# Performance work log

Hardware: AMD Instinct MI355X
Metric: run time of the kernel (lower is better)

## Reference

```python
import jax, jax.numpy as jnp
import numpy as np

NUM_EMB = 16384
EMB_DIM = 64
BETA = 0.25  # commitment_cost, legacy=True formulation


def _l2norm(x, axis=-1):
    # matches F.normalize(p=2): x / max(||x||, 1e-12)
    n = jnp.sqrt(jnp.sum(x * x, axis=axis, keepdims=True))
    return x / jnp.maximum(n, 1e-12)


def setup_inputs() -> dict:
    key = jax.random.key(0)
    k_z, k_cb, k_w, k_b = jax.random.split(key, 4)
    z = jax.random.normal(k_z, (16, 1024, EMB_DIM), dtype=jnp.float32)
    # frozen codebook: N(0, d^{-0.5})
    codebook = jax.random.normal(k_cb, (NUM_EMB, EMB_DIM), dtype=jnp.float32) * (EMB_DIM ** -0.5)
    # Linear(d, d) default init: U(-1/sqrt(d), 1/sqrt(d))
    lim = 1.0 / np.sqrt(EMB_DIM)
    proj_w = jax.random.uniform(k_w, (EMB_DIM, EMB_DIM), dtype=jnp.float32, minval=-lim, maxval=lim)
    proj_b = jax.random.uniform(k_b, (EMB_DIM,), dtype=jnp.float32, minval=-lim, maxval=lim)
    scale = jnp.float32(10.0)  # l2_norm_scale
    return {"z": z, "codebook": codebook, "proj_w": proj_w, "proj_b": proj_b, "scale": scale}


def reference(z, codebook, proj_w, proj_b, scale):
    B, T, d = z.shape
    zf = z.reshape(-1, d)                                   # [BT, d]
    quant_codebook = codebook @ proj_w.T + proj_b           # [N, d]
    zn = _l2norm(zf)
    cn = _l2norm(quant_codebook)
    distances = -jnp.einsum('bd,nd->bn', zn, cn) * scale    # [BT, N]
    idx = jnp.argmin(distances, axis=1)                     # [BT]
    quantized = quant_codebook[idx].reshape(z.shape)        # [B, T, d]
    sg = jax.lax.stop_gradient
    commitment_loss = jnp.mean((sg(quantized) - z) ** 2)
    codebook_loss = jnp.mean((quantized - sg(z)) ** 2)
    vq_loss = commitment_loss + BETA * codebook_loss        # legacy=True
    quantized_st = z + sg(quantized - z)                    # straight-through
    return quantized_st, vq_loss, idx.reshape(B, T)
```

## Files before the change

### kernel.cpp

```cpp
#include <hip/hip_runtime.h>
#include <hip/hip_bf16.h>


#define NCODES 16384
#define NTOK   16384
#define DIM    64
#define MARGIN_MFMA 8e-3f
#define CAP    16

typedef __attribute__((ext_vector_type(8))) short bf16x8;
typedef __attribute__((ext_vector_type(4))) float f32x4;
#define GLOBAL_AS __attribute__((address_space(1)))
#define LDS_AS    __attribute__((address_space(3)))

__device__ float  g_qcb[NCODES * DIM];
__device__ short  g_cnb[NCODES * DIM];
__device__ short  g_znb[NTOK * DIM];
__device__ unsigned g_topu[NTOK];
__device__ int    g_candcnt[NTOK];
__device__ int    g_cand[NTOK * CAP];
__device__ int    g_wl[NTOK];
__device__ int    g_wln;
__device__ float  g_partial[512];

__device__ __forceinline__ float wave_sum64(float v) {
#pragma unroll
  for (int o = 32; o > 0; o >>= 1) v += __shfl_xor(v, o, 64);
  return v;
}
__device__ __forceinline__ short f2bf(float f) {
  __hip_bfloat16 h = __float2bfloat16(f);
  return *reinterpret_cast<short*>(&h);
}
__device__ __forceinline__ float bf2f(short s) {
  __hip_bfloat16 h = *reinterpret_cast<__hip_bfloat16*>(&s);
  return __bfloat162float(h);
}
__device__ __forceinline__ void split8(const float* v, bf16x8& hi, bf16x8& lo) {
#pragma unroll
  for (int i = 0; i < 8; ++i) {
    float f = v[i];
    short h = f2bf(f);
    hi[i] = h;
    lo[i] = f2bf(f - bf2f(h));
  }
}

__global__ __launch_bounds__(256) void k_prep(const float* __restrict__ cb,
                                              const float* __restrict__ pw,
                                              const float* __restrict__ pb,
                                              const float* __restrict__ z) {
  int tid = threadIdx.x;
  int wave = tid >> 6, lane = tid & 63, quad = lane >> 4, col = lane & 15;
  if (blockIdx.x < 256) {
    int rowBase = blockIdx.x * 64 + wave * 16;
    const float* cr = cb + (size_t)(rowBase + col) * 64 + quad * 8;
    bf16x8 ah0, al0, ah1, al1;
    split8(cr, ah0, al0);
    split8(cr + 32, ah1, al1);
    float vals[4][4];
    float nr[4] = {0.f, 0.f, 0.f, 0.f};
    const f32x4 fz = {0.f, 0.f, 0.f, 0.f};
#pragma unroll
    for (int nt = 0; nt < 4; ++nt) {
      int j = col + 16 * nt;
      const float* wr = pw + (size_t)j * 64 + quad * 8;
      bf16x8 bh0, bl0, bh1, bl1;
      split8(wr, bh0, bl0);
      split8(wr + 32, bh1, bl1);
      f32x4 d = __builtin_amdgcn_mfma_f32_16x16x32_bf16(ah0, bh0, fz, 0, 0, 0);
      d = __builtin_amdgcn_mfma_f32_16x16x32_bf16(ah1, bh1, d, 0, 0, 0);
      d = __builtin_amdgcn_mfma_f32_16x16x32_bf16(ah0, bl0, d, 0, 0, 0);
      d = __builtin_amdgcn_mfma_f32_16x16x32_bf16(ah1, bl1, d, 0, 0, 0);
      d = __builtin_amdgcn_mfma_f32_16x16x32_bf16(al0, bh0, d, 0, 0, 0);
      d = __builtin_amdgcn_mfma_f32_16x16x32_bf16(al1, bh1, d, 0, 0, 0);
      float bj = pb[j];
#pragma unroll
      for (int r = 0; r < 4; ++r) {
        float v = d[r] + bj;
        vals[nt][r] = v;
        nr[r] = fmaf(v, v, nr[r]);
      }
    }
#pragma unroll
    for (int r = 0; r < 4; ++r) {
      float v = nr[r];
      v += __shfl_xor(v, 1, 64);
      v += __shfl_xor(v, 2, 64);
      v += __shfl_xor(v, 4, 64);
      v += __shfl_xor(v, 8, 64);
      nr[r] = 1.0f / fmaxf(sqrtf(v), 1e-12f);
    }
#pragma unroll
    for (int nt = 0; nt < 4; ++nt)
#pragma unroll
      for (int r = 0; r < 4; ++r) {
        int row = rowBase + quad * 4 + r;
        int j = col + 16 * nt;
        g_qcb[(size_t)row * 64 + j] = vals[nt][r];
        g_cnb[(size_t)row * 64 + j] = f2bf(vals[nt][r] * nr[r]);
      }
  } else {
    int zb = blockIdx.x - 256;
    int gid = zb * 256 + tid;
    if (gid < NTOK) { g_topu[gid] = 0u; g_candcnt[gid] = 0; }
    if (gid == 0) g_wln = 0;
    int base = zb * 64;
    for (int r = 0; r < 16; ++r) {
      int row = base + wave * 16 + r;
      float v = z[(size_t)row * 64 + lane];
      float tot = wave_sum64(v * v);
      g_znb[(size_t)row * 64 + lane] = f2bf(v / fmaxf(sqrtf(tot), 1e-12f));
    }
  }
}

__global__ __launch_bounds__(256) void k_mfma1() {
  __shared__ __align__(16) short smB[2][8192];
  int tid = threadIdx.x;
  int wave = tid >> 6, lane = tid & 63;
  int quad = lane >> 4, col = lane & 15;
  int tokBlock = blockIdx.x >> 3, split = blockIdx.x & 7;
  int tokBase = tokBlock * 128 + wave * 32;

  const short* za = g_znb + (size_t)(tokBase + col) * 64 + quad * 8;
  bf16x8 A0[2], A1[2];
#pragma unroll
  for (int f = 0; f < 2; ++f) {
    A0[f] = *(const bf16x8*)(za + f * 16 * 64);
    A1[f] = *(const bf16x8*)(za + f * 16 * 64 + 32);
  }
  float m[2][4];
#pragma unroll
  for (int f = 0; f < 2; ++f)
#pragma unroll
    for (int r = 0; r < 4; ++r) m[f][r] = -3.0e38f;

  const char* gsplit = (const char*)(g_cnb + (size_t)split * 2048 * 64);
  int x = col & 7;
  int s0off = ((quad ^ x) << 3);
  int s1off = (((4 | quad) ^ x) << 3);
  int goff[4];
#pragma unroll
  for (int i = 0; i < 4; ++i) {
    int cidx = wave * 256 + i * 64 + lane;
    int row = cidx >> 3, sw = cidx & 7;
    goff[i] = row * 128 + ((sw ^ (row & 7)) << 4);
  }

#pragma unroll
  for (int i = 0; i < 4; ++i)
    __builtin_amdgcn_global_load_lds((const GLOBAL_AS void*)(gsplit + goff[i]),
                                     (LDS_AS void*)(&smB[0][wave * 2048 + i * 512]), 16, 0, 0);
  __syncthreads();

  int p = 0;
  for (int s = 0; s < 16; ++s) {
    if (s < 15) {
      const char* gb = gsplit + (size_t)(s + 1) * 16384;
#pragma unroll
      for (int i = 0; i < 4; ++i)
        __builtin_amdgcn_global_load_lds((const GLOBAL_AS void*)(gb + goff[i]),
                                         (LDS_AS void*)(&smB[p ^ 1][wave * 2048 + i * 512]),
                                         16, 0, 0);
    }
    const short* bufp = smB[p];
#pragma unroll
    for (int h = 0; h < 2; ++h) {
      bf16x8 B0[4], B1[4];
#pragma unroll
      for (int t = 0; t < 4; ++t) {
        const short* lb = bufp + ((h * 4 + t) * 16 + col) * 64;
        B0[t] = *(const bf16x8*)(lb + s0off);
        B1[t] = *(const bf16x8*)(lb + s1off);
      }
#pragma unroll
      for (int t = 0; t < 4; ++t) {
#pragma unroll
        for (int f = 0; f < 2; ++f) {
          f32x4 acc = {0.f, 0.f, 0.f, 0.f};
          acc = __builtin_amdgcn_mfma_f32_16x16x32_bf16(A0[f], B0[t], acc, 0, 0, 0);
          acc = __builtin_amdgcn_mfma_f32_16x16x32_bf16(A1[f], B1[t], acc, 0, 0, 0);
#pragma unroll
          for (int r = 0; r < 4; ++r) m[f][r] = fmaxf(m[f][r], acc[r]);
        }
      }
    }
    __syncthreads();
    p ^= 1;
  }

#pragma unroll
  for (int f = 0; f < 2; ++f)
#pragma unroll
    for (int r = 0; r < 4; ++r) {
      float v = m[f][r];
      v = fmaxf(v, __shfl_xor(v, 1, 64));
      v = fmaxf(v, __shfl_xor(v, 2, 64));
      v = fmaxf(v, __shfl_xor(v, 4, 64));
      v = fmaxf(v, __shfl_xor(v, 8, 64));
      if (col == 0) {
        unsigned b = __float_as_uint(v);
        unsigned e = (b & 0x80000000u) ? ~b : (b | 0x80000000u);
        atomicMax(&g_topu[tokBase + f * 16 + quad * 4 + r], e);
      }
    }
}

__global__ __launch_bounds__(256) void k_mfma2() {
  __shared__ __align__(16) short smB[2][8192];
  int tid = threadIdx.x;
  int wave = tid >> 6, lane = tid & 63;
  int quad = lane >> 4, col = lane & 15;
  int tokBlock = blockIdx.x >> 3, split = blockIdx.x & 7;
  int tokBase = tokBlock * 128 + wave * 32;

  const short* za = g_znb + (size_t)(tokBase + col) * 64 + quad * 8;
  bf16x8 A0[2], A1[2];
#pragma unroll
  for (int f = 0; f < 2; ++f) {
    A0[f] = *(const bf16x8*)(za + f * 16 * 64);
    A1[f] = *(const bf16x8*)(za + f * 16 * 64 + 32);
  }
  float th[2][4];
#pragma unroll
  for (int f = 0; f < 2; ++f)
#pragma unroll
    for (int r = 0; r < 4; ++r) {
      unsigned u = g_topu[tokBase + f * 16 + quad * 4 + r];
      unsigned b = (u & 0x80000000u) ? (u & 0x7FFFFFFFu) : ~u;
      th[f][r] = __uint_as_float(b) - MARGIN_MFMA;
    }

  const char* gsplit = (const char*)(g_cnb + (size_t)split * 2048 * 64);
  int x = col & 7;
  int s0off = ((quad ^ x) << 3);
  int s1off = (((4 | quad) ^ x) << 3);
  int goff[4];
#pragma unroll
  for (int i = 0; i < 4; ++i) {
    int cidx = wave * 256 + i * 64 + lane;
    int row = cidx >> 3, sw = cidx & 7;
    goff[i] = row * 128 + ((sw ^ (row & 7)) << 4);
  }

#pragma unroll
  for (int i = 0; i < 4; ++i)
    __builtin_amdgcn_global_load_lds((const GLOBAL_AS void*)(gsplit + goff[i]),
                                     (LDS_AS void*)(&smB[0][wave * 2048 + i * 512]), 16, 0, 0);
  __syncthreads();

  int codeB = split * 2048 + col;
  int p = 0;
  for (int s = 0; s < 16; ++s) {
    if (s < 15) {
      const char* gb = gsplit + (size_t)(s + 1) * 16384;
#pragma unroll
      for (int i = 0; i < 4; ++i)
        __builtin_amdgcn_global_load_lds((const GLOBAL_AS void*)(gb + goff[i]),
                                         (LDS_AS void*)(&smB[p ^ 1][wave * 2048 + i * 512]),
                                         16, 0, 0);
    }
    const short* bufp = smB[p];
#pragma unroll
    for (int h = 0; h < 2; ++h) {
      bf16x8 B0[4], B1[4];
#pragma unroll
      for (int t = 0; t < 4; ++t) {
        const short* lb = bufp + ((h * 4 + t) * 16 + col) * 64;
        B0[t] = *(const bf16x8*)(lb + s0off);
        B1[t] = *(const bf16x8*)(lb + s1off);
      }
#pragma unroll
      for (int t = 0; t < 4; ++t) {
        int code = codeB + s * 128 + (h * 4 + t) * 16;
#pragma unroll
        for (int f = 0; f < 2; ++f) {
          f32x4 acc = {0.f, 0.f, 0.f, 0.f};
          acc = __builtin_amdgcn_mfma_f32_16x16x32_bf16(A0[f], B0[t], acc, 0, 0, 0);
          acc = __builtin_amdgcn_mfma_f32_16x16x32_bf16(A1[f], B1[t], acc, 0, 0, 0);
          float dmax = fmaxf(fmaxf(acc[0] - th[f][0], acc[1] - th[f][1]),
                             fmaxf(acc[2] - th[f][2], acc[3] - th[f][3]));
          if (dmax >= 0.f) {
#pragma unroll
            for (int r = 0; r < 4; ++r) {
              if (acc[r] >= th[f][r]) {
                int tok = tokBase + f * 16 + quad * 4 + r;
                int pos = atomicAdd(&g_candcnt[tok], 1);
                if (pos < CAP) g_cand[tok * CAP + pos] = code;
              }
            }
          }
        }
      }
    }
    __syncthreads();
    p ^= 1;
  }
}

__global__ __launch_bounds__(256) void k_scan() {
  __shared__ int flags[256];
  __shared__ int sbase;
  int tid = threadIdx.x;
  int tok = blockIdx.x * 256 + tid;
  int flag = (g_candcnt[tok] >= 2) ? 1 : 0;
  flags[tid] = flag;
  __syncthreads();
  if (tid == 0) {
    int run = 0;
    for (int i = 0; i < 256; ++i) {
      int f = flags[i];
      flags[i] = run;
      run += f;
    }
    sbase = atomicAdd(&g_wln, run);
  }
  __syncthreads();
  if (flag) g_wl[sbase + flags[tid]] = tok;
}

__global__ __launch_bounds__(256) void k_arb(const float* __restrict__ z,
                                             const float* __restrict__ cb,
                                             const float* __restrict__ pw,
                                             const float* __restrict__ pb) {
  __shared__ double WT[64 * 65];
  __shared__ float cbl[4][64];
  int tid = threadIdx.x;
  int wave = tid >> 6, lane = tid & 63;
  for (int e = tid; e < 4096; e += 256) {
    int j = e >> 6, k = e & 63;
    WT[k * 65 + j] = (double)pw[e];
  }
  __syncthreads();

  int wln = g_wln;
  double bj = (double)pb[lane];
  int gwave = blockIdx.x * 4 + wave;

  for (int e = gwave; e < wln; e += 1024) {
    int tok = g_wl[e];
    int cnt = g_candcnt[tok];
    double zj = (double)z[(size_t)tok * 64 + lane];
    double best = -1.0e300;
    int bi = 0x7FFFFFFF;
    int lim = (cnt <= CAP) ? cnt : 0;
    for (int c = 0; c < lim; ++c) {
      int code = g_cand[tok * CAP + c];
      cbl[wave][lane] = cb[(size_t)code * 64 + lane];
      double s0 = 0.0, s1 = 0.0, s2 = 0.0, s3 = 0.0;
#pragma unroll
      for (int kk = 0; kk < 16; ++kk) {
        s0 = fma(WT[kk * 65 + lane], (double)cbl[wave][kk], s0);
        s1 = fma(WT[(kk + 16) * 65 + lane], (double)cbl[wave][kk + 16], s1);
        s2 = fma(WT[(kk + 32) * 65 + lane], (double)cbl[wave][kk + 32], s2);
        s3 = fma(WT[(kk + 48) * 65 + lane], (double)cbl[wave][kk + 48], s3);
      }
      double qc = ((s0 + s1) + (s2 + s3)) + bj;
      double s = zj * qc, n2 = qc * qc;
#pragma unroll
      for (int o = 32; o > 0; o >>= 1) {
        s += __shfl_xor(s, o, 64);
        n2 += __shfl_xor(n2, o, 64);
      }
      double key = s / fmax(sqrt(n2), 1e-12);
      if (key > best || (key == best && code < bi)) { best = key; bi = code; }
    }
    if (cnt > CAP) {
      for (int code = 0; code < NCODES; ++code) {
        cbl[wave][lane] = cb[(size_t)code * 64 + lane];
        double s0 = 0.0, s1 = 0.0, s2 = 0.0, s3 = 0.0;
#pragma unroll
        for (int kk = 0; kk < 16; ++kk) {
          s0 = fma(WT[kk * 65 + lane], (double)cbl[wave][kk], s0);
          s1 = fma(WT[(kk + 16) * 65 + lane], (double)cbl[wave][kk + 16], s1);
          s2 = fma(WT[(kk + 32) * 65 + lane], (double)cbl[wave][kk + 32], s2);
          s3 = fma(WT[(kk + 48) * 65 + lane], (double)cbl[wave][kk + 48], s3);
        }
        double qc = ((s0 + s1) + (s2 + s3)) + bj;
        double s = zj * qc, n2 = qc * qc;
#pragma unroll
        for (int o = 32; o > 0; o >>= 1) {
          s += __shfl_xor(s, o, 64);
          n2 += __shfl_xor(n2, o, 64);
        }
        double key = s / fmax(sqrt(n2), 1e-12);
        if (key > best || (key == best && code < bi)) { best = key; bi = code; }
      }
    }
    if (lane == 0) g_cand[tok * CAP] = bi;
  }
}

__global__ __launch_bounds__(256) void k_out(const float* __restrict__ z,
                                             float* __restrict__ out0,
                                             float* __restrict__ out2) {
  __shared__ float ws[4];
  int tid = threadIdx.x;
  int wave = tid >> 6, lane = tid & 63;
  int base = blockIdx.x * 32;
  float lsum = 0.f;
  for (int r = 0; r < 8; ++r) {
    int tok = base + wave * 8 + r;
    int idx = g_cand[tok * CAP];
    float q = g_qcb[(size_t)idx * 64 + lane];
    float zv = z[(size_t)tok * 64 + lane];
    float d = q - zv;
    out0[(size_t)tok * 64 + lane] = zv + d;
    lsum = fmaf(d, d, lsum);
    if (lane == 0) out2[tok] = (float)idx;
  }
  float tot = wave_sum64(lsum);
  if (lane == 0) ws[wave] = tot;
  __syncthreads();
  if (tid == 0) g_partial[blockIdx.x] = ((ws[0] + ws[1]) + (ws[2] + ws[3]));
}

__global__ void k_loss(float* __restrict__ out1) {
  int lane = threadIdx.x;
  float s = 0.f;
#pragma unroll
  for (int i = 0; i < 8; ++i) s += g_partial[lane + 64 * i];
  s = wave_sum64(s);
  if (lane == 0) out1[0] = 1.25f * s / 1048576.0f;
}

extern "C" void kernel_launch(void* const* d_in, const int* in_sizes, int n_in,
                              void* d_out, int out_size, void* d_ws, size_t ws_size,
                              hipStream_t stream) {
  const float* z = (const float*)d_in[0];
  const float* cb = (const float*)d_in[1];
  const float* pw = (const float*)d_in[2];
  const float* pb = (const float*)d_in[3];

  float* out0 = (float*)d_out;
  float* out1 = out0 + (size_t)NTOK * DIM;
  float* out2 = out1 + 1;

  hipLaunchKernelGGL(k_prep, dim3(512), dim3(256), 0, stream, cb, pw, pb, z);
  hipLaunchKernelGGL(k_mfma1, dim3(1024), dim3(256), 0, stream);
  hipLaunchKernelGGL(k_mfma2, dim3(1024), dim3(256), 0, stream);
  hipLaunchKernelGGL(k_scan, dim3(64), dim3(256), 0, stream);
  hipLaunchKernelGGL(k_arb, dim3(256), dim3(256), 0, stream, z, cb, pw, pb);
  hipLaunchKernelGGL(k_out, dim3(512), dim3(256), 0, stream, z, out0, out2);
  hipLaunchKernelGGL(k_loss, dim3(1), dim3(64), 0, stream, out1);
}
```

Before: 202.0 us.

## Record per-stage max scores and skip stages below threshold in second pass

The first MFMA pass now reduces the max similarity for each 128-code stage per token and writes it to a global buffer, in addition to the global max. The second pass loads these stage maxima and skips the MFMA recompute for any stage and 16-token fragment where no token's stage max reaches the threshold. This removes most of the redundant second-pass matmul work. In exchange the first pass does more shuffle reductions and global writes per stage, an 8 MB scratch buffer is added, and the second pass gains divergent control flow.

```diff
diff --git a/kernel.cpp b/kernel.cpp
--- a/kernel.cpp
+++ b/kernel.cpp
@@ -17,6 +17,7 @@
 __device__ short  g_cnb[NCODES * DIM];
 __device__ short  g_znb[NTOK * DIM];
 __device__ unsigned g_topu[NTOK];
+__device__ float  g_stgmax[128 * NTOK];
 __device__ int    g_candcnt[NTOK];
 __device__ int    g_cand[NTOK * CAP];
 __device__ int    g_wl[NTOK];
@@ -165,6 +166,11 @@
                                          16, 0, 0);
     }
     const short* bufp = smB[p];
+    float st[2][4];
+#pragma unroll
+    for (int f = 0; f < 2; ++f)
+#pragma unroll
+      for (int r = 0; r < 4; ++r) st[f][r] = -3.0e38f;
 #pragma unroll
     for (int h = 0; h < 2; ++h) {
       bf16x8 B0[4], B1[4];
@@ -182,10 +188,24 @@
           acc = __builtin_amdgcn_mfma_f32_16x16x32_bf16(A0[f], B0[t], acc, 0, 0, 0);
           acc = __builtin_amdgcn_mfma_f32_16x16x32_bf16(A1[f], B1[t], acc, 0, 0, 0);
 #pragma unroll
-          for (int r = 0; r < 4; ++r) m[f][r] = fmaxf(m[f][r], acc[r]);
+          for (int r = 0; r < 4; ++r) st[f][r] = fmaxf(st[f][r], acc[r]);
         }
       }
     }
+    int sg = split * 16 + s;
+#pragma unroll
+    for (int f = 0; f < 2; ++f)
+#pragma unroll
+      for (int r = 0; r < 4; ++r) {
+        float v = st[f][r];
+        v = fmaxf(v, __shfl_xor(v, 1, 64));
+        v = fmaxf(v, __shfl_xor(v, 2, 64));
+        v = fmaxf(v, __shfl_xor(v, 4, 64));
+        v = fmaxf(v, __shfl_xor(v, 8, 64));
+        m[f][r] = fmaxf(m[f][r], v);
+        if (col == 0)
+          g_stgmax[(size_t)sg * NTOK + tokBase + f * 16 + quad * 4 + r] = v;
+      }
     __syncthreads();
     p ^= 1;
   }
@@ -194,13 +214,8 @@
   for (int f = 0; f < 2; ++f)
 #pragma unroll
     for (int r = 0; r < 4; ++r) {
-      float v = m[f][r];
-      v = fmaxf(v, __shfl_xor(v, 1, 64));
-      v = fmaxf(v, __shfl_xor(v, 2, 64));
-      v = fmaxf(v, __shfl_xor(v, 4, 64));
-      v = fmaxf(v, __shfl_xor(v, 8, 64));
       if (col == 0) {
-        unsigned b = __float_as_uint(v);
+        unsigned b = __float_as_uint(m[f][r]);
         unsigned e = (b & 0x80000000u) ? ~b : (b | 0x80000000u);
         atomicMax(&g_topu[tokBase + f * 16 + quad * 4 + r], e);
       }
@@ -231,6 +246,12 @@
       unsigned b = (u & 0x80000000u) ? (u & 0x7FFFFFFFu) : ~u;
       th[f][r] = __uint_as_float(b) - MARGIN_MFMA;
     }
+  float thlin;
+  {
+    unsigned u = g_topu[tokBase + (lane & 31)];
+    unsigned b = (u & 0x80000000u) ? (u & 0x7FFFFFFFu) : ~u;
+    thlin = __uint_as_float(b) - MARGIN_MFMA;
+  }
 
   const char* gsplit = (const char*)(g_cnb + (size_t)split * 2048 * 64);
   int x = col & 7;
@@ -248,6 +269,7 @@
   for (int i = 0; i < 4; ++i)
     __builtin_amdgcn_global_load_lds((const GLOBAL_AS void*)(gsplit + goff[i]),
                                      (LDS_AS void*)(&smB[0][wave * 2048 + i * 512]), 16, 0, 0);
+  float sv = g_stgmax[(size_t)(split * 16) * NTOK + tokBase + (lane & 31)];
   __syncthreads();
 
   int codeB = split * 2048 + col;
@@ -261,33 +283,61 @@
                                          (LDS_AS void*)(&smB[p ^ 1][wave * 2048 + i * 512]),
                                          16, 0, 0);
     }
-    const short* bufp = smB[p];
-#pragma unroll
-    for (int h = 0; h < 2; ++h) {
-      bf16x8 B0[4], B1[4];
-#pragma unroll
-      for (int t = 0; t < 4; ++t) {
-        const short* lb = bufp + ((h * 4 + t) * 16 + col) * 64;
-        B0[t] = *(const bf16x8*)(lb + s0off);
-        B1[t] = *(const bf16x8*)(lb + s1off);
-      }
-#pragma unroll
-      for (int t = 0; t < 4; ++t) {
-        int code = codeB + s * 128 + (h * 4 + t) * 16;
-#pragma unroll
-        for (int f = 0; f < 2; ++f) {
-          f32x4 acc = {0.f, 0.f, 0.f, 0.f};
-          acc = __builtin_amdgcn_mfma_f32_16x16x32_bf16(A0[f], B0[t], acc, 0, 0, 0);
-          acc = __builtin_amdgcn_mfma_f32_16x16x32_bf16(A1[f], B1[t], acc, 0, 0, 0);
-          float dmax = fmaxf(fmaxf(acc[0] - th[f][0], acc[1] - th[f][1]),
-                             fmaxf(acc[2] - th[f][2], acc[3] - th[f][3]));
-          if (dmax >= 0.f) {
-#pragma unroll
-            for (int r = 0; r < 4; ++r) {
-              if (acc[r] >= th[f][r]) {
-                int tok = tokBase + f * 16 + quad * 4 + r;
-                int pos = atomicAdd(&g_candcnt[tok], 1);
-                if (pos < CAP) g_cand[tok * CAP + pos] = code;
+    int nd = (sv >= thlin) ? 1 : 0;
+    nd |= __shfl_xor(nd, 1, 64);
+    nd |= __shfl_xor(nd, 2, 64);
+    nd |= __shfl_xor(nd, 4, 64);
+    nd |= __shfl_xor(nd, 8, 64);
+    int f0n = __shfl(nd, 0, 64);
+    int f1n = __shfl(nd, 16, 64);
+    if (s < 15)
+      sv = g_stgmax[(size_t)(split * 16 + s + 1) * NTOK + tokBase + (lane & 31)];
+
+    if (f0n | f1n) {
+      const short* bufp = smB[p];
+#pragma unroll
+      for (int h = 0; h < 2; ++h) {
+        bf16x8 B0[4], B1[4];
+#pragma unroll
+        for (int t = 0; t < 4; ++t) {
+          const short* lb = bufp + ((h * 4 + t) * 16 + col) * 64;
+          B0[t] = *(const bf16x8*)(lb + s0off);
+          B1[t] = *(const bf16x8*)(lb + s1off);
+        }
+#pragma unroll
+        for (int t = 0; t < 4; ++t) {
+          int code = codeB + s * 128 + (h * 4 + t) * 16;
+          if (f0n) {
+            f32x4 acc = {0.f, 0.f, 0.f, 0.f};
+            acc = __builtin_amdgcn_mfma_f32_16x16x32_bf16(A0[0], B0[t], acc, 0, 0, 0);
+            acc = __builtin_amdgcn_mfma_f32_16x16x32_bf16(A1[0], B1[t], acc, 0, 0, 0);
+            float dmax = fmaxf(fmaxf(acc[0] - th[0][0], acc[1] - th[0][1]),
+                               fmaxf(acc[2] - th[0][2], acc[3] - th[0][3]));
+            if (dmax >= 0.f) {
+#pragma unroll
+              for (int r = 0; r < 4; ++r) {
+                if (acc[r] >= th[0][r]) {
+                  int tok = tokBase + quad * 4 + r;
+                  int pos = atomicAdd(&g_candcnt[tok], 1);
+                  if (pos < CAP) g_cand[tok * CAP + pos] = code;
+                }
+              }
+            }
+          }
+          if (f1n) {
+            f32x4 acc = {0.f, 0.f, 0.f, 0.f};
+            acc = __builtin_amdgcn_mfma_f32_16x16x32_bf16(A0[1], B0[t], acc, 0, 0, 0);
+            acc = __builtin_amdgcn_mfma_f32_16x16x32_bf16(A1[1], B1[t], acc, 0, 0, 0);
+            float dmax = fmaxf(fmaxf(acc[0] - th[1][0], acc[1] - th[1][1]),
+                               fmaxf(acc[2] - th[1][2], acc[3] - th[1][3]));
+            if (dmax >= 0.f) {
+#pragma unroll
+              for (int r = 0; r < 4; ++r) {
+                if (acc[r] >= th[1][r]) {
+                  int tok = tokBase + 16 + quad * 4 + r;
+                  int pos = atomicAdd(&g_candcnt[tok], 1);
+                  if (pos < CAP) g_cand[tok * CAP + pos] = code;
+                }
               }
             }
           }
```

New measurement: 238.7 us. +18.1%, slower.
